# Kernel tuning notes

Measured on AMD Instinct MI355X. Metric: run time of the kernel, lower is better.

The kernel has to match this reference:

```python
import jax, jax.numpy as jnp
import numpy as np

N = 50000      # nodes
E = 250000     # edges
IN = 256       # in_channels
OUT = 256      # out_channels
H = 4          # heads
C = OUT // H   # per-head channels = 64
MSG = 128
TIME = 64
ED = MSG + TIME + 2   # edge_dim = 194


def _glorot(k, shape):
    return (jax.random.normal(k, shape, jnp.float32) / np.sqrt(shape[0])).astype(jnp.float32)


def setup_inputs() -> dict:
    ks = jax.random.split(jax.random.key(0), 16)
    z = lambda: jnp.zeros((H * C,), jnp.float32)
    inp = {
        "x": jax.random.normal(ks[0], (N, IN), jnp.float32),
        "edge_index": jax.random.randint(ks[1], (2, E), 0, N),
        "edge_attr": jax.random.normal(ks[2], (E, ED), jnp.float32),
        # conv1 params (in_channels=IN)
        "Wq1": _glorot(ks[3], (IN, H * C)), "bq1": z(),
        "Wk1": _glorot(ks[4], (IN, H * C)), "bk1": z(),
        "Wv1": _glorot(ks[5], (IN, H * C)), "bv1": z(),
        "We1": _glorot(ks[6], (ED, H * C)),              # lin_edge has no bias in PyG
        "Ws1": _glorot(ks[7], (IN, H * C)), "bs1": z(),  # skip/root connection
        # conv2 params (in_channels=OUT)
        "Wq2": _glorot(ks[8], (OUT, H * C)), "bq2": z(),
        "Wk2": _glorot(ks[9], (OUT, H * C)), "bk2": z(),
        "Wv2": _glorot(ks[10], (OUT, H * C)), "bv2": z(),
        "We2": _glorot(ks[11], (ED, H * C)),
        "Ws2": _glorot(ks[12], (OUT, H * C)), "bs2": z(),
    }
    return inp


def _tconv(x, src, dst, edge_attr, Wq, bq, Wk, bk, Wv, bv, We, Ws, bs):
    """PyG TransformerConv (heads=H, concat=True, root_weight=True), eval mode."""
    n = x.shape[0]
    q = (x @ Wq + bq).reshape(n, H, C)
    k = (x @ Wk + bk).reshape(n, H, C)
    v = (x @ Wv + bv).reshape(n, H, C)
    e = (edge_attr @ We).reshape(-1, H, C)          # [E,H,C]
    kj = k[src] + e                                  # key + edge embedding
    vj = v[src] + e                                  # value + edge embedding
    logits = jnp.einsum('ehc,ehc->eh', q[dst], kj) / np.sqrt(C)  # [E,H]
    # segment softmax over incoming edges of each dst node
    m = jax.lax.stop_gradient(jax.ops.segment_max(logits, dst, num_segments=n))
    ex = jnp.exp(logits - m[dst])
    denom = jax.ops.segment_sum(ex, dst, num_segments=n)
    a = ex / (denom[dst] + 1e-16)                    # [E,H]
    agg = jax.ops.segment_sum(vj * a[:, :, None], dst, num_segments=n)  # [N,H,C]
    return agg.reshape(n, H * C) + x @ Ws + bs


def reference(x, edge_index, edge_attr,
              Wq1, bq1, Wk1, bk1, Wv1, bv1, We1, Ws1, bs1,
              Wq2, bq2, Wk2, bk2, Wv2, bv2, We2, Ws2, bs2):
    src, dst = edge_index[0], edge_index[1]
    h = jax.nn.relu(_tconv(x, src, dst, edge_attr,
                           Wq1, bq1, Wk1, bk1, Wv1, bv1, We1, Ws1, bs1))
    # dropout is identity in eval mode
    return _tconv(h, src, dst, edge_attr,
                  Wq2, bq2, Wk2, bk2, Wv2, bv2, We2, Ws2, bs2)
```

## Files before the change

### kernel.cpp

```cpp
#include <hip/hip_runtime.h>

#define N_NODES 50000
#define N_EDGES 250000
#define DIM 256
#define ED 194
#define EDP 224
#define MP_NODE 50048
#define MP_EDGE 250112

typedef __bf16 bf16x8 __attribute__((ext_vector_type(8)));
typedef float f32x4 __attribute__((ext_vector_type(4)));
typedef short s16x8 __attribute__((ext_vector_type(8)));
typedef short s16x4 __attribute__((ext_vector_type(4)));
typedef unsigned short u16x8 __attribute__((ext_vector_type(8)));

__device__ __forceinline__ float bf2f(unsigned short b){
  union { unsigned int u; float f; } v; v.u = ((unsigned int)b)<<16; return v.f;
}
__device__ __forceinline__ short f2bf(float f){
  union { float f; unsigned int u; } v; v.f = f;
  unsigned int u = v.u;
  return (short)((u + 0x7fffu + ((u>>16)&1u))>>16);
}

__device__ __forceinline__ void gload_lds16(const void* g, void* l){
  __builtin_amdgcn_global_load_lds(
      (const __attribute__((address_space(1))) unsigned int*)g,
      (__attribute__((address_space(3))) unsigned int*)l, 16, 0, 0);
}

__global__ __launch_bounds__(256) void convert_x_kernel(
    const float* __restrict__ x, short* __restrict__ xb)
{
  int idx = blockIdx.x*256 + threadIdx.x;
  s16x4 o;
  if (idx < N_NODES*64){
    float4 a = *(const float4*)(x + (size_t)idx*4);
    o[0]=f2bf(a.x); o[1]=f2bf(a.y); o[2]=f2bf(a.z); o[3]=f2bf(a.w);
  } else {
    o[0]=0; o[1]=0; o[2]=0; o[3]=0;
  }
  *(s16x4*)(xb + (size_t)idx*4) = o;
}

#define E_ROWS 32
__global__ __launch_bounds__(256) void convert_e_kernel(
    const float* __restrict__ ea, short* __restrict__ eb)
{
  __shared__ float lds[E_ROWS*ED];
  int row0 = blockIdx.x * E_ROWS;
  int tid = threadIdx.x;
  int base = row0 * ED;
  int valid = N_EDGES*ED - base;

  for (int i = tid; i < E_ROWS*ED/4; i += 256){
    float4 v;
    if (i*4 < valid) v = *(const float4*)(ea + base + i*4);
    else             v = make_float4(0.f,0.f,0.f,0.f);
    *(float4*)(lds + i*4) = v;
  }
  __syncthreads();

  for (int u = tid; u < E_ROWS*28; u += 256){
    int row = u / 28;
    int c8  = u - row*28;
    int col = c8*8;
    s16x8 o;
    if (col + 8 <= ED){
      #pragma unroll
      for (int j2=0;j2<4;j2++){
        float2 f = *(const float2*)(lds + row*ED + col + j2*2);
        o[j2*2]   = f2bf(f.x);
        o[j2*2+1] = f2bf(f.y);
      }
    } else {
      #pragma unroll
      for (int j=0;j<8;j++){
        int c = col + j;
        o[j] = (c < ED) ? f2bf(lds[row*ED + c]) : (short)0;
      }
    }
    *(s16x8*)(eb + (size_t)(row0+row)*EDP + col) = o;
  }
}

__global__ __launch_bounds__(256) void transpose_node_w(
    const float* __restrict__ Wq, const float* __restrict__ Wk,
    const float* __restrict__ Wv, const float* __restrict__ Ws,
    short* __restrict__ WtN)
{
  int idx = blockIdx.x*256 + threadIdx.x;
  int w = idx>>16, rem = idx&65535;
  int i = rem>>8, o = rem&255;
  const float* W = (w==0)?Wq:((w==1)?Wk:((w==2)?Wv:Ws));
  WtN[(w<<16) + o*256 + i] = f2bf(W[i*256+o]);
}
__global__ __launch_bounds__(256) void bias_cat_kernel(
    const float* __restrict__ b0, const float* __restrict__ b1,
    const float* __restrict__ b2, const float* __restrict__ b3,
    float* __restrict__ biasN)
{
  int t = blockIdx.x*256 + threadIdx.x;
  const float* b = (t<256)?b0:((t<512)?b1:((t<768)?b2:b3));
  biasN[t] = b[t&255];
}
__global__ __launch_bounds__(256) void transpose_edge_w(
    const float* __restrict__ We, short* __restrict__ WtE)
{
  int idx = blockIdx.x*256 + threadIdx.x;
  int k = idx>>8, o = idx&255;
  WtE[o*EDP + k] = (k<ED) ? f2bf(We[k*256+o]) : (short)0;
}

__global__ __launch_bounds__(256) void zero_ints(int* __restrict__ p, int n){
  int i = blockIdx.x*256 + threadIdx.x;
  if (i<n) p[i] = 0;
}
__global__ __launch_bounds__(256) void count_deg(const int* __restrict__ dst, int* __restrict__ deg){
  int e = blockIdx.x*256 + threadIdx.x;
  if (e < N_EDGES) atomicAdd(&deg[dst[e]], 1);
}
#define SCAN_NBLK 196
__global__ __launch_bounds__(256) void scan_p1(const int* __restrict__ deg, int* __restrict__ part){
  int t = threadIdx.x;
  int i = blockIdx.x*256 + t;
  int v = (i<N_NODES)? deg[i] : 0;
  #pragma unroll
  for (int off=32; off; off>>=1) v += __shfl_xor(v, off, 64);
  __shared__ int s[4];
  if ((t&63)==0) s[t>>6] = v;
  __syncthreads();
  if (t==0) part[blockIdx.x] = s[0]+s[1]+s[2]+s[3];
}
__global__ __launch_bounds__(256) void scan_p2(int* __restrict__ part){
  __shared__ int s[256];
  int t = threadIdx.x;
  int v = (t<SCAN_NBLK)? part[t] : 0;
  s[t] = v; __syncthreads();
  for (int off=1; off<256; off<<=1){
    int x = (t>=off)? s[t-off] : 0;
    __syncthreads();
    s[t] += x;
    __syncthreads();
  }
  part[t] = (t==0)? 0 : s[t-1];
}
__global__ __launch_bounds__(256) void scan_p3(const int* __restrict__ deg,
    const int* __restrict__ part, int* __restrict__ rowptr, int* __restrict__ cursor){
  __shared__ int s[256];
  int t = threadIdx.x;
  int i = blockIdx.x*256 + t;
  int v = (i<N_NODES)? deg[i] : 0;
  s[t] = v; __syncthreads();
  for (int off=1; off<256; off<<=1){
    int x = (t>=off)? s[t-off] : 0;
    __syncthreads();
    s[t] += x;
    __syncthreads();
  }
  if (i < N_NODES){ rowptr[i+1] = part[blockIdx.x] + s[t]; cursor[i] = 0; }
  if (i == 0) rowptr[0] = 0;
}
__global__ __launch_bounds__(256) void scatter_edges(
    const int* __restrict__ src, const int* __restrict__ dst,
    const int* __restrict__ rowptr, int* __restrict__ cursor, int2* __restrict__ csr)
{
  int e = blockIdx.x*256 + threadIdx.x;
  if (e < N_EDGES){
    int d = dst[e];
    int pos = atomicAdd(&cursor[d], 1);
    csr[rowptr[d] + pos] = make_int2(src[e]<<11, e<<9);
  }
}

template<int K, int NLD, bool HAS_BIAS>
__global__ __launch_bounds__(256) void gemm_bt(
    const short* __restrict__ A, const short* __restrict__ Bt,
    const float* __restrict__ bias, short* __restrict__ out, int M)
{
  __shared__ short As[128*32];
  __shared__ short Bs[128*32];
  int tid = threadIdx.x;
  int lane = tid & 63, wave = tid >> 6;
  int m0 = blockIdx.x*128, n0 = blockIdx.y*128;

  int srow = tid>>2, scol = (tid&3)*8;
  const short* gA = A + (size_t)(m0+srow)*K + scol;
  const short* gB = Bt + (size_t)(n0+srow)*K + scol;
  short* ldsA1 = As + wave*512;
  short* ldsA2 = As + 2048 + wave*512;
  short* ldsB1 = Bs + wave*512;
  short* ldsB2 = Bs + 2048 + wave*512;

  int wr = wave>>1, wc = wave&1;
  int fr = lane & 15;
  int kq = lane >> 4;
  f32x4 acc[4][4];
  #pragma unroll
  for (int a=0;a<4;a++)
    #pragma unroll
    for (int b=0;b<4;b++) acc[a][b] = (f32x4){0.f,0.f,0.f,0.f};

  for (int k0=0; k0<K; k0+=32){
    __syncthreads();
    gload_lds16(gA + k0,                ldsA1);
    gload_lds16(gA + (size_t)64*K + k0, ldsA2);
    gload_lds16(gB + k0,                ldsB1);
    gload_lds16(gB + (size_t)64*K + k0, ldsB2);
    __syncthreads();

    bf16x8 af[4], bf[4];
    const short* ar = As + (wr*64 + fr)*32 + kq*8;
    const short* br = Bs + (wc*64 + fr)*32 + kq*8;
    #pragma unroll
    for (int fm=0;fm<4;fm++) af[fm] = *(const bf16x8*)(ar + fm*512);
    #pragma unroll
    for (int fn=0;fn<4;fn++) bf[fn] = *(const bf16x8*)(br + fn*512);
    #pragma unroll
    for (int fm=0;fm<4;fm++)
      #pragma unroll
      for (int fn=0;fn<4;fn++)
        acc[fm][fn] = __builtin_amdgcn_mfma_f32_16x16x32_bf16(af[fm], bf[fn], acc[fm][fn], 0, 0, 0);
  }

  int cr = (lane>>4)*4;
  int cc = lane & 15;
  #pragma unroll
  for (int fm=0;fm<4;fm++){
    #pragma unroll
    for (int fn=0;fn<4;fn++){
      int col = n0 + wc*64 + fn*16 + cc;
      float bv = HAS_BIAS ? bias[col] : 0.f;
      #pragma unroll
      for (int i=0;i<4;i++){
        int row = m0 + wr*64 + fm*16 + cr + i;
        if (row < M) out[(size_t)row*NLD + col] = f2bf(acc[fm][fn][i] + bv);
      }
    }
  }
}

__global__ __launch_bounds__(256) void edge_phase_kernel(
    const short* __restrict__ QKVS, const short* __restrict__ Eemb,
    const int* __restrict__ rowptr, const int2* __restrict__ csr,
    short* __restrict__ out_bf, float* __restrict__ out_f, int relu)
{
  int tid = threadIdx.x, wave = tid>>6, lane = tid&63;
  int node = blockIdx.x*4 + wave;
  if (node >= N_NODES){
    if (node < MP_NODE && out_bf){
      s16x4 z; z[0]=0; z[1]=0; z[2]=0; z[3]=0;
      *(s16x4*)(out_bf + (size_t)node*256 + lane*4) = z;
    }
    return;
  }
  int half = lane>>5;
  int hl   = lane&31;
  int c8   = hl*8;
  const unsigned short* base = (const unsigned short*)QKVS + (size_t)node*1024;

  u16x8 qu = *(const u16x8*)(base + c8);
  float q[8];
  #pragma unroll
  for (int j=0;j<8;j++) q[j] = bf2f(qu[j])*0.125f;

  int beg = rowptr[node], end = rowptr[node+1];
  float l = 0.f;
  float a[8];
  #pragma unroll
  for (int j=0;j<8;j++) a[j] = 0.f;
  int kb = 512 + hl*16;
  int ebo = hl*16;

  for (int idx = beg; idx < end; idx += 2){
    int j = idx + half;
    int jc = (j < end) ? j : (end-1);
    int2 se = csr[jc];
    const char* Kp = (const char*)QKVS + (unsigned)(se.x + kb);
    const char* Ep = (const char*)Eemb + (unsigned)(se.y + ebo);
    u16x8 ku = *(const u16x8*)Kp;
    u16x8 vu = *(const u16x8*)(Kp + 512);
    u16x8 eu = *(const u16x8*)Ep;
    float vv[8];
    float t = 0.f;
    #pragma unroll
    for (int c=0;c<8;c++){
      float ef = bf2f(eu[c]);
      float kf = bf2f(ku[c]) + ef;
      vv[c]    = bf2f(vu[c]) + ef;
      t += q[c]*kf;
    }
    t += __shfl_xor(t, 1, 64);
    t += __shfl_xor(t, 2, 64);
    t += __shfl_xor(t, 4, 64);
    float p = (j < end) ? __expf(t) : 0.f;
    l += p;
    #pragma unroll
    for (int c=0;c<8;c++) a[c] += p*vv[c];
  }

  l += __shfl_xor(l, 32, 64);
  #pragma unroll
  for (int c=0;c<8;c++) a[c] += __shfl_xor(a[c], 32, 64);

  float inv = (l > 0.f) ? 1.0f/l : 0.f;
  u16x8 su = *(const u16x8*)(base + 768 + c8);
  float r[8];
  #pragma unroll
  for (int c=0;c<8;c++){
    float v = a[c]*inv + bf2f(su[c]);
    r[c] = relu ? fmaxf(v, 0.f) : v;
  }

  if (out_bf){
    if (!half){
      s16x8 o;
      #pragma unroll
      for (int c=0;c<8;c++) o[c] = f2bf(r[c]);
      *(s16x8*)(out_bf + (size_t)node*256 + c8) = o;
    }
  } else {
    float4 st = half ? make_float4(r[4],r[5],r[6],r[7])
                     : make_float4(r[0],r[1],r[2],r[3]);
    *(float4*)(out_f + (size_t)node*256 + c8 + half*4) = st;
  }
}

extern "C" void kernel_launch(void* const* d_in, const int* in_sizes, int n_in,
                              void* d_out, int out_size, void* d_ws, size_t ws_size,
                              hipStream_t stream)
{
  const float* x     = (const float*)d_in[0];
  const int*   eidx  = (const int*)d_in[1];
  const float* eattr = (const float*)d_in[2];
  const float* Wq1=(const float*)d_in[3],  *bq1=(const float*)d_in[4];
  const float* Wk1=(const float*)d_in[5],  *bk1=(const float*)d_in[6];
  const float* Wv1=(const float*)d_in[7],  *bv1=(const float*)d_in[8];
  const float* We1=(const float*)d_in[9];
  const float* Ws1=(const float*)d_in[10], *bs1=(const float*)d_in[11];
  const float* Wq2=(const float*)d_in[12], *bq2=(const float*)d_in[13];
  const float* Wk2=(const float*)d_in[14], *bk2=(const float*)d_in[15];
  const float* Wv2=(const float*)d_in[16], *bv2=(const float*)d_in[17];
  const float* We2=(const float*)d_in[18];
  const float* Ws2=(const float*)d_in[19], *bs2=(const float*)d_in[20];

  char* ws = (char*)d_ws;
  size_t off = 0;
  auto alloc = [&](size_t bytes)->char*{
    char* p = ws + off; off = (off + bytes + 255) & ~(size_t)255; return p;
  };
  short* QKVS  = (short*)alloc((size_t)N_NODES*1024*2);
  short* Eemb  = (short*)alloc((size_t)N_EDGES*256*2);
  short* x_bf  = (short*)alloc((size_t)MP_NODE*DIM*2);
  short* h_bf  = (short*)alloc((size_t)MP_NODE*DIM*2);
  short* e_bf  = (short*)alloc((size_t)MP_EDGE*EDP*2);
  short* WtN   = (short*)alloc((size_t)4*65536*2);
  short* WtE   = (short*)alloc((size_t)256*EDP*2);
  float* biasN = (float*)alloc((size_t)1024*4);
  int*   deg   = (int*)alloc((size_t)N_NODES*4);
  int*   rowptr= (int*)alloc((size_t)(N_NODES+1)*4);
  int*   cursor= (int*)alloc((size_t)N_NODES*4);
  int*   part  = (int*)alloc((size_t)256*4);
  int2*  csr   = (int2*)alloc((size_t)N_EDGES*8);

  const int* srcp = eidx;
  const int* dstp = eidx + N_EDGES;

  const int EB = (N_EDGES + 255)/256;
  const int NB = (N_NODES + 255)/256;

  convert_x_kernel<<<MP_NODE*64/256,256,0,stream>>>(x, x_bf);
  convert_e_kernel<<<MP_EDGE/E_ROWS,256,0,stream>>>(eattr, e_bf);

  zero_ints<<<NB,256,0,stream>>>(deg, N_NODES);
  count_deg<<<EB,256,0,stream>>>(dstp, deg);
  scan_p1<<<SCAN_NBLK,256,0,stream>>>(deg, part);
  scan_p2<<<1,256,0,stream>>>(part);
  scan_p3<<<SCAN_NBLK,256,0,stream>>>(deg, part, rowptr, cursor);
  scatter_edges<<<EB,256,0,stream>>>(srcp, dstp, rowptr, cursor, csr);

  transpose_node_w<<<1024,256,0,stream>>>(Wq1,Wk1,Wv1,Ws1,WtN);
  bias_cat_kernel<<<4,256,0,stream>>>(bq1,bk1,bv1,bs1,biasN);
  transpose_edge_w<<<224,256,0,stream>>>(We1,WtE);
  gemm_bt<DIM,1024,true><<<dim3(MP_NODE/128,8),256,0,stream>>>(x_bf, WtN, biasN, QKVS, N_NODES);
  gemm_bt<EDP,256,false><<<dim3(MP_EDGE/128,2),256,0,stream>>>(e_bf, WtE, nullptr, Eemb, N_EDGES);
  edge_phase_kernel<<<MP_NODE/4,256,0,stream>>>(QKVS,Eemb,rowptr,csr,h_bf,nullptr,1);

  transpose_node_w<<<1024,256,0,stream>>>(Wq2,Wk2,Wv2,Ws2,WtN);
  bias_cat_kernel<<<4,256,0,stream>>>(bq2,bk2,bv2,bs2,biasN);
  transpose_edge_w<<<224,256,0,stream>>>(We2,WtE);
  gemm_bt<DIM,1024,true><<<dim3(MP_NODE/128,8),256,0,stream>>>(h_bf, WtN, biasN, QKVS, N_NODES);
  gemm_bt<EDP,256,false><<<dim3(MP_EDGE/128,2),256,0,stream>>>(e_bf, WtE, nullptr, Eemb, N_EDGES);
  edge_phase_kernel<<<N_NODES/4,256,0,stream>>>(QKVS,Eemb,rowptr,csr,nullptr,(float*)d_out,0);
}
```

Measured before the change: 877.6 us.

## Fuse weight prep kernels, fold degree zeroing, unroll edge loop by two

```diff
diff --git a/kernel.cpp b/kernel.cpp
--- a/kernel.cpp
+++ b/kernel.cpp
@@ -30,9 +30,10 @@
 }
 
 __global__ __launch_bounds__(256) void convert_x_kernel(
-    const float* __restrict__ x, short* __restrict__ xb)
+    const float* __restrict__ x, short* __restrict__ xb, int* __restrict__ deg)
 {
   int idx = blockIdx.x*256 + threadIdx.x;
+  if (idx < N_NODES) deg[idx] = 0;
   s16x4 o;
   if (idx < N_NODES*64){
     float4 a = *(const float4*)(x + (size_t)idx*4);
@@ -84,38 +85,62 @@
   }
 }
 
-__global__ __launch_bounds__(256) void transpose_node_w(
+__global__ __launch_bounds__(256) void prep_weights(
     const float* __restrict__ Wq, const float* __restrict__ Wk,
     const float* __restrict__ Wv, const float* __restrict__ Ws,
-    short* __restrict__ WtN)
-{
-  int idx = blockIdx.x*256 + threadIdx.x;
-  int w = idx>>16, rem = idx&65535;
-  int i = rem>>8, o = rem&255;
-  const float* W = (w==0)?Wq:((w==1)?Wk:((w==2)?Wv:Ws));
-  WtN[(w<<16) + o*256 + i] = f2bf(W[i*256+o]);
-}
-__global__ __launch_bounds__(256) void bias_cat_kernel(
+    const float* __restrict__ We,
     const float* __restrict__ b0, const float* __restrict__ b1,
     const float* __restrict__ b2, const float* __restrict__ b3,
-    float* __restrict__ biasN)
-{
-  int t = blockIdx.x*256 + threadIdx.x;
-  const float* b = (t<256)?b0:((t<512)?b1:((t<768)?b2:b3));
-  biasN[t] = b[t&255];
-}
-__global__ __launch_bounds__(256) void transpose_edge_w(
-    const float* __restrict__ We, short* __restrict__ WtE)
-{
-  int idx = blockIdx.x*256 + threadIdx.x;
-  int k = idx>>8, o = idx&255;
-  WtE[o*EDP + k] = (k<ED) ? f2bf(We[k*256+o]) : (short)0;
-}
-
-__global__ __launch_bounds__(256) void zero_ints(int* __restrict__ p, int n){
-  int i = blockIdx.x*256 + threadIdx.x;
-  if (i<n) p[i] = 0;
-}
+    short* __restrict__ WtN, short* __restrict__ WtE, float* __restrict__ biasN)
+{
+  __shared__ short lds[64*65];
+  int b = blockIdx.x, tid = threadIdx.x;
+  if (b < 64){
+    int mat = b>>4, tile = b&15;
+    int i0 = (tile>>2)*64, o0 = (tile&3)*64;
+    const float* W = (mat==0)?Wq:((mat==1)?Wk:((mat==2)?Wv:Ws));
+    #pragma unroll
+    for (int t=0;t<16;t++){
+      int idx = t*256+tid; int r = idx>>6, c = idx&63;
+      lds[r*65+c] = f2bf(W[(size_t)(i0+r)*256 + o0 + c]);
+    }
+    __syncthreads();
+    #pragma unroll
+    for (int t=0;t<4;t++){
+      int idx = t*256+tid; int r = idx>>4, c4 = (idx&15)*4;
+      s16x4 o;
+      o[0]=lds[(c4+0)*65+r]; o[1]=lds[(c4+1)*65+r];
+      o[2]=lds[(c4+2)*65+r]; o[3]=lds[(c4+3)*65+r];
+      *(s16x4*)(WtN + (mat<<16) + (o0+r)*256 + i0 + c4) = o;
+    }
+  } else if (b < 80){
+    int b2 = b-64;
+    int k0 = (b2>>2)*64, o0 = (b2&3)*64;
+    #pragma unroll
+    for (int t=0;t<16;t++){
+      int idx = t*256+tid; int r = idx>>6, c = idx&63;
+      int k = k0+r;
+      lds[r*65+c] = (k<ED) ? f2bf(We[(size_t)k*256 + o0 + c]) : (short)0;
+    }
+    __syncthreads();
+    #pragma unroll
+    for (int t=0;t<4;t++){
+      int idx = t*256+tid; int r = idx>>4, c4 = (idx&15)*4;
+      if (k0 + c4 < EDP){
+        s16x4 o;
+        o[0]=lds[(c4+0)*65+r]; o[1]=lds[(c4+1)*65+r];
+        o[2]=lds[(c4+2)*65+r]; o[3]=lds[(c4+3)*65+r];
+        *(s16x4*)(WtE + (o0+r)*EDP + k0 + c4) = o;
+      }
+    }
+  } else {
+    for (int t = tid; t < 1024; t += 256){
+      const float* bb = (t<256)?b0:((t<512)?b1:((t<768)?b2:b3));
+      biasN[t] = bb[t&255];
+    }
+  }
+}
+
 __global__ __launch_bounds__(256) void count_deg(const int* __restrict__ dst, int* __restrict__ deg){
   int e = blockIdx.x*256 + threadIdx.x;
   if (e < N_EDGES) atomicAdd(&deg[dst[e]], 1);
@@ -265,6 +290,7 @@
   for (int j=0;j<8;j++) q[j] = bf2f(qu[j])*0.125f;
 
   int beg = rowptr[node], end = rowptr[node+1];
+  int last = end - 1;
   float l = 0.f;
   float a[8];
   #pragma unroll
@@ -272,31 +298,44 @@
   int kb = 512 + hl*16;
   int ebo = hl*16;
 
-  for (int idx = beg; idx < end; idx += 2){
-    int j = idx + half;
-    int jc = (j < end) ? j : (end-1);
-    int2 se = csr[jc];
-    const char* Kp = (const char*)QKVS + (unsigned)(se.x + kb);
-    const char* Ep = (const char*)Eemb + (unsigned)(se.y + ebo);
-    u16x8 ku = *(const u16x8*)Kp;
-    u16x8 vu = *(const u16x8*)(Kp + 512);
-    u16x8 eu = *(const u16x8*)Ep;
-    float vv[8];
-    float t = 0.f;
+  for (int idx = beg; idx < end; idx += 4){
+    int j0 = idx + half;
+    int j1 = idx + 2 + half;
+    int jc0 = (j0 < end) ? j0 : last;
+    int jc1 = (j1 < end) ? j1 : last;
+    int2 se0 = csr[jc0];
+    int2 se1 = csr[jc1];
+    const char* Kp0 = (const char*)QKVS + (unsigned)(se0.x + kb);
+    const char* Ep0 = (const char*)Eemb + (unsigned)(se0.y + ebo);
+    const char* Kp1 = (const char*)QKVS + (unsigned)(se1.x + kb);
+    const char* Ep1 = (const char*)Eemb + (unsigned)(se1.y + ebo);
+    u16x8 ku0 = *(const u16x8*)Kp0;
+    u16x8 vu0 = *(const u16x8*)(Kp0 + 512);
+    u16x8 eu0 = *(const u16x8*)Ep0;
+    u16x8 ku1 = *(const u16x8*)Kp1;
+    u16x8 vu1 = *(const u16x8*)(Kp1 + 512);
+    u16x8 eu1 = *(const u16x8*)Ep1;
+    float vv0[8], vv1[8];
+    float t0 = 0.f, t1 = 0.f;
     #pragma unroll
     for (int c=0;c<8;c++){
-      float ef = bf2f(eu[c]);
-      float kf = bf2f(ku[c]) + ef;
-      vv[c]    = bf2f(vu[c]) + ef;
-      t += q[c]*kf;
-    }
-    t += __shfl_xor(t, 1, 64);
-    t += __shfl_xor(t, 2, 64);
-    t += __shfl_xor(t, 4, 64);
-    float p = (j < end) ? __expf(t) : 0.f;
-    l += p;
-    #pragma unroll
-    for (int c=0;c<8;c++) a[c] += p*vv[c];
+      float ef0 = bf2f(eu0[c]);
+      float kf0 = bf2f(ku0[c]) + ef0;
+      vv0[c]    = bf2f(vu0[c]) + ef0;
+      t0 += q[c]*kf0;
+      float ef1 = bf2f(eu1[c]);
+      float kf1 = bf2f(ku1[c]) + ef1;
+      vv1[c]    = bf2f(vu1[c]) + ef1;
+      t1 += q[c]*kf1;
+    }
+    t0 += __shfl_xor(t0, 1, 64);  t1 += __shfl_xor(t1, 1, 64);
+    t0 += __shfl_xor(t0, 2, 64);  t1 += __shfl_xor(t1, 2, 64);
+    t0 += __shfl_xor(t0, 4, 64);  t1 += __shfl_xor(t1, 4, 64);
+    float p0 = (j0 < end) ? __expf(t0) : 0.f;
+    float p1 = (j1 < end) ? __expf(t1) : 0.f;
+    l += p0 + p1;
+    #pragma unroll
+    for (int c=0;c<8;c++) a[c] += p0*vv0[c] + p1*vv1[c];
   }
 
   l += __shfl_xor(l, 32, 64);
@@ -367,28 +406,22 @@
   const int* dstp = eidx + N_EDGES;
 
   const int EB = (N_EDGES + 255)/256;
-  const int NB = (N_NODES + 255)/256;
-
-  convert_x_kernel<<<MP_NODE*64/256,256,0,stream>>>(x, x_bf);
+
+  convert_x_kernel<<<MP_NODE*64/256,256,0,stream>>>(x, x_bf, deg);
   convert_e_kernel<<<MP_EDGE/E_ROWS,256,0,stream>>>(eattr, e_bf);
 
-  zero_ints<<<NB,256,0,stream>>>(deg, N_NODES);
   count_deg<<<EB,256,0,stream>>>(dstp, deg);
   scan_p1<<<SCAN_NBLK,256,0,stream>>>(deg, part);
   scan_p2<<<1,256,0,stream>>>(part);
   scan_p3<<<SCAN_NBLK,256,0,stream>>>(deg, part, rowptr, cursor);
   scatter_edges<<<EB,256,0,stream>>>(srcp, dstp, rowptr, cursor, csr);
 
-  transpose_node_w<<<1024,256,0,stream>>>(Wq1,Wk1,Wv1,Ws1,WtN);
-  bias_cat_kernel<<<4,256,0,stream>>>(bq1,bk1,bv1,bs1,biasN);
-  transpose_edge_w<<<224,256,0,stream>>>(We1,WtE);
+  prep_weights<<<81,256,0,stream>>>(Wq1,Wk1,Wv1,Ws1,We1,bq1,bk1,bv1,bs1,WtN,WtE,biasN);
   gemm_bt<DIM,1024,true><<<dim3(MP_NODE/128,8),256,0,stream>>>(x_bf, WtN, biasN, QKVS, N_NODES);
   gemm_bt<EDP,256,false><<<dim3(MP_EDGE/128,2),256,0,stream>>>(e_bf, WtE, nullptr, Eemb, N_EDGES);
   edge_phase_kernel<<<MP_NODE/4,256,0,stream>>>(QKVS,Eemb,rowptr,csr,h_bf,nullptr,1);
 
-  transpose_node_w<<<1024,256,0,stream>>>(Wq2,Wk2,Wv2,Ws2,WtN);
-  bias_cat_kernel<<<4,256,0,stream>>>(bq2,bk2,bv2,bs2,biasN);
-  transpose_edge_w<<<224,256,0,stream>>>(We2,WtE);
+  prep_weights<<<81,256,0,stream>>>(Wq2,Wk2,Wv2,Ws2,We2,bq2,bk2,bv2,bs2,WtN,WtE,biasN);
   gemm_bt<DIM,1024,true><<<dim3(MP_NODE/128,8),256,0,stream>>>(h_bf, WtN, biasN, QKVS, N_NODES);
   gemm_bt<EDP,256,false><<<dim3(MP_EDGE/128,2),256,0,stream>>>(e_bf, WtE, nullptr, Eemb, N_EDGES);
   edge_phase_kernel<<<N_NODES/4,256,0,stream>>>(QKVS,Eemb,rowptr,csr,nullptr,(float*)d_out,0);
```

Measured after the change: 889.9 us. About the same (+1.4%).
